# Kernel tuning notes

Measured on AMD Instinct MI355X. Metric: run time of the kernel, lower is better.

Reference implementation:

```python
import jax, jax.numpy as jnp
import numpy as np

B, S, D, H, DFF, E = 8, 1024, 1024, 16, 4096, 16
T = B * S
C = (2 * T) // E  # top-2 capacity, capacity_factor_eff = 1.0
EPS = 1.1920929e-07


def setup_inputs() -> dict:
    key = jax.random.key(0)
    ks = jax.random.split(key, 16)
    r = lambda k, shape, sc: jax.random.normal(k, shape, dtype=jnp.float32) * sc
    return {
        "x": r(ks[0], (B, S, D), 1.0),
        "in_proj_w": r(ks[1], (3 * D, D), 0.02),
        "in_proj_b": jnp.zeros((3 * D,), jnp.float32),
        "out_proj_w": r(ks[2], (D, D), 0.02),
        "out_proj_b": jnp.zeros((D,), jnp.float32),
        "ln1_g": jnp.ones((D,), jnp.float32),
        "ln1_b": jnp.zeros((D,), jnp.float32),
        "ln2_g": jnp.ones((D,), jnp.float32),
        "ln2_b": jnp.zeros((D,), jnp.float32),
        "wg": r(ks[3], (D, E), 0.02),
        "w1": r(ks[4], (E, D, DFF), 0.02),
        "b1": jnp.zeros((E, DFF), jnp.float32),
        "w2": r(ks[5], (E, DFF, D), 0.02),
        "b2": jnp.zeros((E, D), jnp.float32),
    }


def _layernorm(v, g, b):
    m = v.mean(-1, keepdims=True)
    var = ((v - m) ** 2).mean(-1, keepdims=True)
    return (v - m) * jax.lax.rsqrt(var + 1e-5) * g + b


def reference(x, in_proj_w, in_proj_b, out_proj_w, out_proj_b,
              ln1_g, ln1_b, ln2_g, ln2_b, wg, w1, b1, w2, b2):
    hd = D // H
    # ---- self-attention block (dropout=0, eval) ----
    qkv = x @ in_proj_w.T + in_proj_b          # [B,S,3D]
    q, k, v = jnp.split(qkv, 3, axis=-1)
    heads = lambda t: t.reshape(B, S, H, hd).transpose(0, 2, 1, 3)  # [B,H,S,hd]
    q, k, v = heads(q), heads(k), heads(v)
    att = jax.nn.softmax(jnp.einsum('bhqd,bhkd->bhqk', q, k) / np.float32(np.sqrt(hd)), axis=-1)
    o = jnp.einsum('bhqk,bhkd->bhqd', att, v).transpose(0, 2, 1, 3).reshape(B, S, D)
    o = o @ out_proj_w.T + out_proj_b
    x = _layernorm(x + o, ln1_g, ln1_b)
    # ---- top-2 MoE (GShard/deepspeed-style gating, no noise at eval) ----
    xt = x.reshape(T, D)
    logits = xt @ wg                                    # [T,E]
    gates = jax.nn.softmax(logits, axis=-1)
    idx1 = jnp.argmax(gates, axis=-1)
    m1 = jax.nn.one_hot(idx1, E, dtype=jnp.float32)
    logits2 = jnp.where(m1 > 0, -jnp.inf, logits)
    idx2 = jnp.argmax(logits2, axis=-1)
    m2 = jax.nn.one_hot(idx2, E, dtype=jnp.float32)
    loc1 = jnp.cumsum(m1, axis=0) - m1                  # position within expert for top-1
    loc2 = jnp.cumsum(m2, axis=0) - m2 + m1.sum(0, keepdims=True)
    m1 = m1 * (loc1 < C)                                # drop tokens over capacity
    m2 = m2 * (loc2 < C)
    p1 = (loc1 * m1).sum(-1).astype(jnp.int32)          # [T] capacity slot
    p2 = (loc2 * m2).sum(-1).astype(jnp.int32)
    g1 = (gates * m1).sum(-1)
    g2 = (gates * m2).sum(-1)
    denom = jnp.maximum(g1 + g2, EPS)
    g1, g2 = g1 / denom, g2 / denom
    keep1 = m1.sum(-1)                                  # 1.0 if kept else 0.0
    keep2 = m2.sum(-1)
    # dispatch: scatter tokens into [E, C, D] expert buffers
    buf = jnp.zeros((E, C, D), x.dtype)
    buf = buf.at[idx1, p1].add(xt * keep1[:, None]).at[idx2, p2].add(xt * keep2[:, None])
    # grouped expert FFN
    h = jax.nn.relu(jnp.einsum('ecd,edh->ech', buf, w1) + b1[:, None, :])
    y = jnp.einsum('ech,ehd->ecd', h, w2) + b2[:, None, :]
    # combine: gather back and weight by normalized gates (zero if dropped)
    moe_out = (g1 * keep1)[:, None] * y[idx1, p1] + (g2 * keep2)[:, None] * y[idx2, p2]
    x = _layernorm(x + moe_out.reshape(B, S, D), ln2_g, ln2_b)
    return x
```

## Files before the change

kernel.cpp:

```cpp
#include <hip/hip_runtime.h>
#include <cstdint>

#define DEVI __device__ __forceinline__

typedef short short8 __attribute__((ext_vector_type(8)));
typedef float f32x4 __attribute__((ext_vector_type(4)));
typedef unsigned short u16;
typedef u16 u16x4 __attribute__((ext_vector_type(4)));

static constexpr int Bz = 8, Ss = 1024, Dd = 1024, Hh = 16, HD = 64, DFF = 4096, Ee = 16;
static constexpr int Tt = Bz * Ss;
static constexpr int Cap = (2 * Tt) / Ee;
static constexpr int D3 = 3 * Dd;
static constexpr float EPSc = 1.1920929e-07f;
static constexpr size_t PT = (size_t)Tt * Dd;

DEVI u16 f2b(float f) {
    union { float f; uint32_t u; } v; v.f = f;
    return (u16)((v.u + 0x7FFFu + ((v.u >> 16) & 1u)) >> 16);
}
DEVI float b2f(u16 h) {
    union { uint32_t u; float f; } v; v.u = ((uint32_t)h) << 16; return v.f;
}
DEVI f32x4 zf4() { f32x4 v; v[0] = 0.f; v[1] = 0.f; v[2] = 0.f; v[3] = 0.f; return v; }

DEVI void gl16(const u16* g, u16* l) {
    __builtin_amdgcn_global_load_lds(
        (const __attribute__((address_space(1))) void*)g,
        (__attribute__((address_space(3))) void*)l, 16, 0, 0);
}

DEVI int swzb(int row, int col) {
    int byte = (row * 64 + col) * 2;
    byte ^= (row & 7) << 4;
    return byte >> 1;
}

__global__ __launch_bounds__(256)
void split3_kernel(const float* __restrict__ in, u16* __restrict__ out, long long n) {
    const long long i = ((long long)blockIdx.x * 256 + threadIdx.x) * 4;
    if (i >= n) return;
    const float4 v = *(const float4*)(in + i);
    const float f[4] = {v.x, v.y, v.z, v.w};
    u16x4 ph, pm, pl;
#pragma unroll
    for (int c = 0; c < 4; ++c) {
        const u16 hi = f2b(f[c]);
        const float r1 = f[c] - b2f(hi);
        const u16 mi = f2b(r1);
        const float r2 = r1 - b2f(mi);
        const u16 lo = f2b(r2);
        ph[c] = hi; pm[c] = mi; pl[c] = lo;
    }
    *(u16x4*)(out + i) = ph;
    *(u16x4*)(out + n + i) = pm;
    *(u16x4*)(out + 2 * n + i) = pl;
}

__global__ __launch_bounds__(256)
void tconv64_kernel(const float* __restrict__ in, u16* __restrict__ out, int R, int Cc) {
    __shared__ u16 tile[64][68];
    const int z = blockIdx.z;
    const int r0 = blockIdx.y * 64, c0 = blockIdx.x * 64;
    const int tr = threadIdx.x >> 4;
    const int tc4 = (threadIdx.x & 15) * 4;
    const float* ip = in + (size_t)z * R * Cc;
#pragma unroll
    for (int i = 0; i < 4; ++i) {
        const int row = tr + i * 16;
        const float4 v = *(const float4*)(ip + (size_t)(r0 + row) * Cc + c0 + tc4);
        u16x4 w;
        w[0] = f2b(v.x); w[1] = f2b(v.y); w[2] = f2b(v.z); w[3] = f2b(v.w);
        *(u16x4*)(&tile[row][tc4]) = w;
    }
    __syncthreads();
    u16* op = out + (size_t)z * R * Cc;
#pragma unroll
    for (int i = 0; i < 4; ++i) {
        const int orow = tr + i * 16;
        u16x4 w;
#pragma unroll
        for (int j = 0; j < 4; ++j) w[j] = tile[tc4 + j][orow];
        *(u16x4*)(op + (size_t)(c0 + orow) * R + r0 + tc4) = w;
    }
}

__global__ __launch_bounds__(256)
void vtrans_kernel(const u16* __restrict__ vh, const u16* __restrict__ vl,
                   u16* __restrict__ vth, u16* __restrict__ vtl) {
    __shared__ u16 th[32][33], tl[32][33];
    const int bh = blockIdx.z, d0 = blockIdx.y * 32, s0 = blockIdx.x * 32;
    const int bb = bh >> 4, hh = bh & 15;
    const int tr = threadIdx.x >> 5, tc = threadIdx.x & 31;
#pragma unroll
    for (int i = 0; i < 4; ++i) {
        const size_t src = (size_t)(bb * Ss + s0 + tr + i * 8) * Dd + hh * HD + d0 + tc;
        th[tr + i * 8][tc] = vh[src];
        tl[tr + i * 8][tc] = vl[src];
    }
    __syncthreads();
#pragma unroll
    for (int i = 0; i < 4; ++i) {
        const size_t dst = ((size_t)bh * HD + d0 + tr + i * 8) * Ss + s0 + tc;
        vth[dst] = th[tc][tr + i * 8];
        vtl[dst] = tl[tc][tr + i * 8];
    }
}

template <int SPLITS, int MODE>
__global__ __launch_bounds__(256)
void gemm_gl(const u16* __restrict__ A, const u16* __restrict__ Bt, void* __restrict__ Cout,
             const float* __restrict__ bias, int M, int N, int K,
             size_t psA, size_t psB,
             u16* __restrict__ qh, u16* __restrict__ ql,
             u16* __restrict__ kh, u16* __restrict__ kl,
             u16* __restrict__ vh, u16* __restrict__ vl) {
    __shared__ u16 As[SPLITS * 128 * 32];
    __shared__ u16 Bs[SPLITS * 128 * 32];
    const int tid = threadIdx.x;
    const int lane = tid & 63, wid = tid >> 6;
    const int wm = wid >> 1, wn = wid & 1;
    const int m0 = blockIdx.y * 128, n0 = blockIdx.x * 128;
    const int lr = lane & 15, lg = lane >> 4;
    const int lrow = lane >> 2;
    const int lcol = (lane & 3) * 8;

    f32x4 acc[4][4];
#pragma unroll
    for (int i = 0; i < 4; ++i)
#pragma unroll
        for (int j = 0; j < 4; ++j) acc[i][j] = zf4();

    for (int kt = 0; kt < K; kt += 32) {
#pragma unroll
        for (int p = 0; p < SPLITS; ++p) {
#pragma unroll
            for (int c = 0; c < 2; ++c) {
                const int r0 = wid * 32 + c * 16;
                gl16(A + p * psA + (size_t)(m0 + r0 + lrow) * K + kt + lcol,
                     As + p * 4096 + r0 * 32 + lane * 8);
                gl16(Bt + p * psB + (size_t)(n0 + r0 + lrow) * K + kt + lcol,
                     Bs + p * 4096 + r0 * 32 + lane * 8);
            }
        }
        __syncthreads();

        short8 af[SPLITS][4];
#pragma unroll
        for (int p = 0; p < SPLITS; ++p)
#pragma unroll
            for (int i = 0; i < 4; ++i)
                af[p][i] = *(const short8*)(As + p * 4096 + (wm * 64 + i * 16 + lr) * 32 + lg * 8);

#pragma unroll
        for (int bp = 0; bp < SPLITS; ++bp) {
            short8 bf[4];
#pragma unroll
            for (int j = 0; j < 4; ++j)
                bf[j] = *(const short8*)(Bs + bp * 4096 + (wn * 64 + j * 16 + lr) * 32 + lg * 8);
#pragma unroll
            for (int ap = 0; ap + bp < SPLITS; ++ap)
#pragma unroll
                for (int i = 0; i < 4; ++i)
#pragma unroll
                    for (int j = 0; j < 4; ++j)
                        acc[i][j] = __builtin_amdgcn_mfma_f32_16x16x32_bf16(af[ap][i], bf[j], acc[i][j], 0, 0, 0);
        }
        __syncthreads();
    }

    const int r4 = lg * 4;
    const int region = n0 >> 10;
#pragma unroll
    for (int j = 0; j < 4; ++j) {
        const int col = n0 + wn * 64 + j * 16 + lr;
        const float bv = bias[col];
#pragma unroll
        for (int i = 0; i < 4; ++i) {
#pragma unroll
            for (int r = 0; r < 4; ++r) {
                const int rowg = m0 + wm * 64 + i * 16 + r4 + r;
                float v = acc[i][j][r] + bv;
                if (MODE == 2) {
                    ((float*)Cout)[(size_t)rowg * N + col] = v;
                } else {
                    const size_t off = (size_t)rowg * Dd + (col & 1023);
                    if (region == 0) {
                        const float fs = v * 0.125f;
                        const u16 h = f2b(fs);
                        qh[off] = h; ql[off] = f2b(fs - b2f(h));
                    } else if (region == 1) {
                        const u16 h = f2b(v);
                        kh[off] = h; kl[off] = f2b(v - b2f(h));
                    } else {
                        const u16 h = f2b(v);
                        vh[off] = h; vl[off] = f2b(v - b2f(h));
                    }
                }
            }
        }
    }
}

template <int RELU>
__global__ __launch_bounds__(512)
void gemm_x2(const u16* __restrict__ A, const u16* __restrict__ Bt, u16* __restrict__ Cout,
             const float* __restrict__ bias, int M, int N, int K,
             size_t sA, size_t sB, size_t sC, int sBias) {
    __shared__ u16 lds[2][2][256 * 64];
    const int tid = threadIdx.x, lane = tid & 63, wid = tid >> 6;
    const int wm = wid >> 2, wn = wid & 3;
    const int lr = lane & 15, lg = lane >> 4;
    const int m0 = blockIdx.y * 256, n0 = blockIdx.x * 256;
    const int e = blockIdx.z;
    const u16* Ab = A + (size_t)e * sA;
    const u16* Bb = Bt + (size_t)e * sB;

    const int srow = wid * 8 + (lane >> 3);
    const int scol = (lane & 7) * 8;

    f32x4 acc[8][4];
#pragma unroll
    for (int i = 0; i < 8; ++i)
#pragma unroll
        for (int j = 0; j < 4; ++j) acc[i][j] = zf4();

#define STAGE_X2(b, kt)                                                              \
    {                                                                                \
        _Pragma("unroll")                                                            \
        for (int c = 0; c < 4; ++c)                                                  \
            gl16(Ab + (size_t)(m0 + c * 64 + srow) * K + (kt) + scol,                \
                 &lds[b][0][(c * 64 + srow) * 64 + scol]);                           \
        _Pragma("unroll")                                                            \
        for (int c = 0; c < 4; ++c)                                                  \
            gl16(Bb + (size_t)(n0 + c * 64 + srow) * K + (kt) + scol,                \
                 &lds[b][1][(c * 64 + srow) * 64 + scol]);                           \
    }

#define COMPUTE_X2(b)                                                                \
    {                                                                                \
        _Pragma("unroll")                                                            \
        for (int ks = 0; ks < 2; ++ks) {                                             \
            short8 af[8], bf[4];                                                     \
            _Pragma("unroll")                                                        \
            for (int i = 0; i < 8; ++i)                                              \
                af[i] = *(const short8*)(&lds[b][0][(wm * 128 + i * 16 + lr) * 64 + ks * 32 + lg * 8]); \
            _Pragma("unroll")                                                        \
            for (int j = 0; j < 4; ++j)                                              \
                bf[j] = *(const short8*)(&lds[b][1][(wn * 64 + j * 16 + lr) * 64 + ks * 32 + lg * 8]);  \
            _Pragma("unroll")                                                        \
            for (int i = 0; i < 8; ++i)                                              \
                _Pragma("unroll")                                                    \
                for (int j = 0; j < 4; ++j)                                          \
                    acc[i][j] = __builtin_amdgcn_mfma_f32_16x16x32_bf16(af[i], bf[j], acc[i][j], 0, 0, 0); \
        }                                                                            \
    }

    const int nt = K >> 6;
    STAGE_X2(0, 0)
    for (int t = 0; t < nt - 1; ++t) {
        const int cur = t & 1;
        STAGE_X2(cur ^ 1, (t + 1) * 64)
        asm volatile("s_waitcnt vmcnt(8)" ::: "memory");
        __builtin_amdgcn_s_barrier();
        COMPUTE_X2(cur)
        asm volatile("s_waitcnt lgkmcnt(0)" ::: "memory");
        __builtin_amdgcn_s_barrier();
    }
    asm volatile("s_waitcnt vmcnt(0)" ::: "memory");
    __builtin_amdgcn_s_barrier();
    COMPUTE_X2((nt - 1) & 1)

#undef STAGE_X2
#undef COMPUTE_X2

    const int r4 = lg * 4;
#pragma unroll
    for (int j = 0; j < 4; ++j) {
        const int col = n0 + wn * 64 + j * 16 + lr;
        const float bv = bias[(size_t)e * sBias + col];
#pragma unroll
        for (int i = 0; i < 8; ++i) {
#pragma unroll
            for (int r = 0; r < 4; ++r) {
                const int rowg = m0 + wm * 128 + i * 16 + r4 + r;
                float v = acc[i][j][r] + bv;
                if (RELU) v = fmaxf(v, 0.f);
                Cout[(size_t)e * sC + (size_t)rowg * N + col] = f2b(v);
            }
        }
    }
}

__global__ __launch_bounds__(256)
void attn_mfma(const u16* __restrict__ qhp, const u16* __restrict__ qlp,
               const u16* __restrict__ khp, const u16* __restrict__ klp,
               const u16* __restrict__ vthp, const u16* __restrict__ vtlp,
               u16* __restrict__ os) {
    __shared__ u16 Khi[64 * 64], Klo[64 * 64];
    __shared__ u16 Vhi[64 * 64], Vlo[64 * 64];
    __shared__ u16 Phi[4][16 * 64], Plo[4][16 * 64];

    const int qt = blockIdx.x, bh = blockIdx.y;
    const int bb = bh >> 4, hh = bh & 15;
    const int tid = threadIdx.x, lane = tid & 63, wid = tid >> 6;
    const int lr = lane & 15, lg = lane >> 4;

    short8 qhi[2], qlo[2];
    {
        const size_t qbase = (size_t)(bb * Ss + qt * 64 + wid * 16 + lr) * Dd + hh * HD;
#pragma unroll
        for (int ks = 0; ks < 2; ++ks) {
            qhi[ks] = *(const short8*)(qhp + qbase + ks * 32 + lg * 8);
            qlo[ks] = *(const short8*)(qlp + qbase + ks * 32 + lg * 8);
        }
    }

    float mrun[4], lrun[4];
    f32x4 oacc[4];
#pragma unroll
    for (int r = 0; r < 4; ++r) { mrun[r] = -1e30f; lrun[r] = 0.f; }
#pragma unroll
    for (int nf = 0; nf < 4; ++nf) oacc[nf] = zf4();

    const int srow = tid >> 2;
    const int sd = (tid & 3) * 16;

    u16* const PhiW = Phi[wid];
    u16* const PloW = Plo[wid];

    for (int kt = 0; kt < Ss / 64; ++kt) {
        const size_t krow = (size_t)(bb * Ss + kt * 64 + srow) * Dd + hh * HD + sd;
        const short8 k0 = *(const short8*)(khp + krow);
        const short8 k1 = *(const short8*)(khp + krow + 8);
        const short8 l0 = *(const short8*)(klp + krow);
        const short8 l1 = *(const short8*)(klp + krow + 8);
        const size_t vrow = ((size_t)bh * HD + srow) * Ss + kt * 64 + sd;
        const short8 v0 = *(const short8*)(vthp + vrow);
        const short8 v1 = *(const short8*)(vthp + vrow + 8);
        const short8 w0 = *(const short8*)(vtlp + vrow);
        const short8 w1 = *(const short8*)(vtlp + vrow + 8);
        __syncthreads();
        *(short8*)(Khi + swzb(srow, sd)) = k0;
        *(short8*)(Khi + swzb(srow, sd + 8)) = k1;
        *(short8*)(Klo + swzb(srow, sd)) = l0;
        *(short8*)(Klo + swzb(srow, sd + 8)) = l1;
        *(short8*)(Vhi + swzb(srow, sd)) = v0;
        *(short8*)(Vhi + swzb(srow, sd + 8)) = v1;
        *(short8*)(Vlo + swzb(srow, sd)) = w0;
        *(short8*)(Vlo + swzb(srow, sd + 8)) = w1;
        __syncthreads();

        f32x4 sc[4];
#pragma unroll
        for (int nf = 0; nf < 4; ++nf) sc[nf] = zf4();
#pragma unroll
        for (int nf = 0; nf < 4; ++nf)
#pragma unroll
            for (int ks = 0; ks < 2; ++ks) {
                const short8 kh = *(const short8*)(Khi + swzb(nf * 16 + lr, ks * 32 + lg * 8));
                const short8 kl = *(const short8*)(Klo + swzb(nf * 16 + lr, ks * 32 + lg * 8));
                sc[nf] = __builtin_amdgcn_mfma_f32_16x16x32_bf16(qhi[ks], kh, sc[nf], 0, 0, 0);
                sc[nf] = __builtin_amdgcn_mfma_f32_16x16x32_bf16(qhi[ks], kl, sc[nf], 0, 0, 0);
                sc[nf] = __builtin_amdgcn_mfma_f32_16x16x32_bf16(qlo[ks], kh, sc[nf], 0, 0, 0);
                sc[nf] = __builtin_amdgcn_mfma_f32_16x16x32_bf16(qlo[ks], kl, sc[nf], 0, 0, 0);
            }

        float scl[4];
#pragma unroll
        for (int r = 0; r < 4; ++r) {
            float m = fmaxf(fmaxf(sc[0][r], sc[1][r]), fmaxf(sc[2][r], sc[3][r]));
            m = fmaxf(m, __shfl_xor(m, 1));
            m = fmaxf(m, __shfl_xor(m, 2));
            m = fmaxf(m, __shfl_xor(m, 4));
            m = fmaxf(m, __shfl_xor(m, 8));
            const float mn = fmaxf(mrun[r], m);
            scl[r] = __expf(mrun[r] - mn);
            mrun[r] = mn;
            float s = 0.f;
#pragma unroll
            for (int nf = 0; nf < 4; ++nf) {
                const float p = __expf(sc[nf][r] - mn);
                sc[nf][r] = p;
                s += p;
            }
            s += __shfl_xor(s, 1);
            s += __shfl_xor(s, 2);
            s += __shfl_xor(s, 4);
            s += __shfl_xor(s, 8);
            lrun[r] = lrun[r] * scl[r] + s;
        }

#pragma unroll
        for (int nf = 0; nf < 4; ++nf)
#pragma unroll
            for (int r = 0; r < 4; ++r) {
                const float p = sc[nf][r];
                const u16 h = f2b(p);
                const int idx = swzb(lg * 4 + r, nf * 16 + lr);
                PhiW[idx] = h;
                PloW[idx] = f2b(p - b2f(h));
            }

#pragma unroll
        for (int nf = 0; nf < 4; ++nf)
#pragma unroll
            for (int r = 0; r < 4; ++r) oacc[nf][r] *= scl[r];

#pragma unroll
        for (int ks = 0; ks < 2; ++ks) {
            const short8 ph = *(const short8*)(PhiW + swzb(lr, ks * 32 + lg * 8));
            const short8 pl = *(const short8*)(PloW + swzb(lr, ks * 32 + lg * 8));
#pragma unroll
            for (int nf = 0; nf < 4; ++nf) {
                const short8 vh = *(const short8*)(Vhi + swzb(nf * 16 + lr, ks * 32 + lg * 8));
                const short8 vl = *(const short8*)(Vlo + swzb(nf * 16 + lr, ks * 32 + lg * 8));
                oacc[nf] = __builtin_amdgcn_mfma_f32_16x16x32_bf16(ph, vh, oacc[nf], 0, 0, 0);
                oacc[nf] = __builtin_amdgcn_mfma_f32_16x16x32_bf16(ph, vl, oacc[nf], 0, 0, 0);
                oacc[nf] = __builtin_amdgcn_mfma_f32_16x16x32_bf16(pl, vh, oacc[nf], 0, 0, 0);
                oacc[nf] = __builtin_amdgcn_mfma_f32_16x16x32_bf16(pl, vl, oacc[nf], 0, 0, 0);
            }
        }
    }

#pragma unroll
    for (int r = 0; r < 4; ++r) {
        const float inv = 1.f / lrun[r];
        const size_t base = (size_t)(bb * Ss + qt * 64 + wid * 16 + lg * 4 + r) * Dd + hh * HD;
#pragma unroll
        for (int nf = 0; nf < 4; ++nf) {
            const float o = oacc[nf][r] * inv;
            const u16 h = f2b(o);
            const float r1 = o - b2f(h);
            const u16 m = f2b(r1);
            const u16 l = f2b(r1 - b2f(m));
            const size_t off = base + nf * 16 + lr;
            os[off] = h;
            os[PT + off] = m;
            os[2 * PT + off] = l;
        }
    }
}

DEVI double block_reduce_d(double v, double* sred, int tid) {
#pragma unroll
    for (int off = 32; off > 0; off >>= 1) v += __shfl_down(v, off);
    __syncthreads();
    if ((tid & 63) == 0) sred[tid >> 6] = v;
    __syncthreads();
    return sred[0] + sred[1] + sred[2] + sred[3];
}

__global__ __launch_bounds__(256)
void ln1_kernel(const float* __restrict__ x, const float* __restrict__ ap,
                const float* __restrict__ g, const float* __restrict__ b,
                float* __restrict__ x1f) {
    __shared__ double sred[4];
    const int t = blockIdx.x, tid = threadIdx.x;
    const float4 xv = ((const float4*)(x + (size_t)t * Dd))[tid];
    const float4 av = ((const float4*)(ap + (size_t)t * Dd))[tid];
    const double v0 = (double)xv.x + (double)av.x;
    const double v1 = (double)xv.y + (double)av.y;
    const double v2 = (double)xv.z + (double)av.z;
    const double v3 = (double)xv.w + (double)av.w;
    const double s = block_reduce_d(v0 + v1 + v2 + v3, sred, tid);
    const double mean = s * (1.0 / Dd);
    const double c0 = v0 - mean, c1 = v1 - mean, c2 = v2 - mean, c3 = v3 - mean;
    const double s2 = block_reduce_d(c0 * c0 + c1 * c1 + c2 * c2 + c3 * c3, sred, tid);
    const double rstd = 1.0 / sqrt(s2 * (1.0 / Dd) + 1e-5);
    const float4 gv = ((const float4*)g)[tid];
    const float4 bv = ((const float4*)b)[tid];
    float4 ov;
    ov.x = (float)(c0 * rstd * (double)gv.x + (double)bv.x);
    ov.y = (float)(c1 * rstd * (double)gv.y + (double)bv.y);
    ov.z = (float)(c2 * rstd * (double)gv.z + (double)bv.z);
    ov.w = (float)(c3 * rstd * (double)gv.w + (double)bv.w);
    ((float4*)(x1f + (size_t)t * Dd))[tid] = ov;
}

__global__ __launch_bounds__(256)
void gate1_kernel(const float* __restrict__ x1f, const float* __restrict__ wg,
                  int* __restrict__ idx1, int* __restrict__ idx2,
                  float* __restrict__ gate1, float* __restrict__ gate2) {
    const int tid = threadIdx.x, lane = tid & 63, wid = tid >> 6;
    const int t = blockIdx.x * 4 + wid;
    double acc[16];
#pragma unroll
    for (int e = 0; e < 16; ++e) acc[e] = 0.0;
    for (int i = 0; i < 16; ++i) {
        const int d = i * 64 + lane;
        const double xv = (double)x1f[(size_t)t * Dd + d];
        const float4* wr = (const float4*)(wg + (size_t)d * 16);
        const float4 w0 = wr[0], w1 = wr[1], w2 = wr[2], w3 = wr[3];
        acc[0] += xv * (double)w0.x;  acc[1] += xv * (double)w0.y;
        acc[2] += xv * (double)w0.z;  acc[3] += xv * (double)w0.w;
        acc[4] += xv * (double)w1.x;  acc[5] += xv * (double)w1.y;
        acc[6] += xv * (double)w1.z;  acc[7] += xv * (double)w1.w;
        acc[8] += xv * (double)w2.x;  acc[9] += xv * (double)w2.y;
        acc[10] += xv * (double)w2.z; acc[11] += xv * (double)w2.w;
        acc[12] += xv * (double)w3.x; acc[13] += xv * (double)w3.y;
        acc[14] += xv * (double)w3.z; acc[15] += xv * (double)w3.w;
    }
#pragma unroll
    for (int e = 0; e < 16; ++e) {
        acc[e] += __shfl_xor(acc[e], 1);
        acc[e] += __shfl_xor(acc[e], 2);
        acc[e] += __shfl_xor(acc[e], 4);
        acc[e] += __shfl_xor(acc[e], 8);
        acc[e] += __shfl_xor(acc[e], 16);
        acc[e] += __shfl_xor(acc[e], 32);
    }
    if (lane == 0) {
        double mx = acc[0];
#pragma unroll
        for (int e = 1; e < 16; ++e) mx = fmax(mx, acc[e]);
        double z = 0.0, ex[16];
#pragma unroll
        for (int e = 0; e < 16; ++e) { ex[e] = exp(acc[e] - mx); z += ex[e]; }
        int b1 = 0; double v1 = acc[0];
#pragma unroll
        for (int e = 1; e < 16; ++e) if (acc[e] > v1) { v1 = acc[e]; b1 = e; }
        int b2 = (b1 == 0) ? 1 : 0; double v2 = acc[b2];
#pragma unroll
        for (int e = 0; e < 16; ++e) if (e != b1 && acc[e] > v2) { v2 = acc[e]; b2 = e; }
        const double rz = 1.0 / z;
        idx1[t] = b1; idx2[t] = b2;
        gate1[t] = (float)(ex[b1] * rz); gate2[t] = (float)(ex[b2] * rz);
    }
}

__global__ __launch_bounds__(256)
void gate2_kernel(const int* __restrict__ idx1, const int* __restrict__ idx2,
                  const float* __restrict__ gate1, const float* __restrict__ gate2,
                  int* __restrict__ p1, int* __restrict__ p2,
                  int* __restrict__ k1, int* __restrict__ k2,
                  float* __restrict__ w1, float* __restrict__ w2) {
    __shared__ int hist[16];
    __shared__ unsigned long long sb1[4][16], sb2[4][16];
    __shared__ int sbase1[16], sbase2[16];
    const int tid = threadIdx.x, lane = tid & 63, wid = tid >> 6;
    if (tid < 16) hist[tid] = 0;
    __syncthreads();
    for (int t = tid; t < Tt; t += 256) atomicAdd(&hist[idx1[t]], 1);
    __syncthreads();
    if (tid < 16) { sbase1[tid] = 0; sbase2[tid] = hist[tid]; }
    __syncthreads();
    const unsigned long long below = (1ULL << lane) - 1ULL;
    for (int ch = 0; ch < Tt / 256; ++ch) {
        const int t = ch * 256 + tid;
        const int a = idx1[t], b = idx2[t];
#pragma unroll
        for (int e = 0; e < 16; ++e) {
            const unsigned long long m1 = __ballot(a == e);
            const unsigned long long m2 = __ballot(b == e);
            if (lane == 0) { sb1[wid][e] = m1; sb2[wid][e] = m2; }
        }
        __syncthreads();
        int r1 = __popcll(sb1[wid][a] & below);
        int r2 = __popcll(sb2[wid][b] & below);
#pragma unroll
        for (int w = 0; w < 4; ++w)
            if (w < wid) { r1 += __popcll(sb1[w][a]); r2 += __popcll(sb2[w][b]); }
        const int loc1 = sbase1[a] + r1, loc2 = sbase2[b] + r2;
        const int kk1 = loc1 < Cap, kk2 = loc2 < Cap;
        const float g1 = kk1 ? gate1[t] : 0.f;
        const float g2 = kk2 ? gate2[t] : 0.f;
        const float dn = fmaxf(g1 + g2, EPSc);
        p1[t] = kk1 ? loc1 : 0;
        p2[t] = kk2 ? loc2 : 0;
        k1[t] = kk1; k2[t] = kk2;
        w1[t] = g1 / dn; w2[t] = g2 / dn;
        __syncthreads();
        if (tid == 0) {
#pragma unroll
            for (int e = 0; e < 16; ++e) {
                int c1 = 0, c2 = 0;
#pragma unroll
                for (int w = 0; w < 4; ++w) { c1 += __popcll(sb1[w][e]); c2 += __popcll(sb2[w][e]); }
                sbase1[e] += c1; sbase2[e] += c2;
            }
        }
        __syncthreads();
    }
}

__global__ __launch_bounds__(256)
void dispatch_kernel(const float* __restrict__ x1f,
                     const int* __restrict__ i1, const int* __restrict__ p1, const int* __restrict__ k1,
                     const int* __restrict__ i2, const int* __restrict__ p2, const int* __restrict__ k2,
                     u16* __restrict__ buf) {
    const int t = blockIdx.x, tid = threadIdx.x;
    const float4 v = ((const float4*)(x1f + (size_t)t * Dd))[tid];
    u16x4 pw;
    pw[0] = f2b(v.x); pw[1] = f2b(v.y); pw[2] = f2b(v.z); pw[3] = f2b(v.w);
    if (k1[t]) *(u16x4*)(buf + ((size_t)i1[t] * Cap + p1[t]) * Dd + tid * 4) = pw;
    if (k2[t]) *(u16x4*)(buf + ((size_t)i2[t] * Cap + p2[t]) * Dd + tid * 4) = pw;
}

__global__ __launch_bounds__(256)
void combine_ln2(const float* __restrict__ x1f, const u16* __restrict__ y,
                 const int* __restrict__ i1, const int* __restrict__ p1, const float* __restrict__ w1,
                 const int* __restrict__ i2, const int* __restrict__ p2, const float* __restrict__ w2,
                 const float* __restrict__ g, const float* __restrict__ b,
                 float* __restrict__ out) {
    __shared__ double sred[4];
    const int t = blockIdx.x, tid = threadIdx.x;
    const size_t r1 = ((size_t)i1[t] * Cap + p1[t]) * Dd;
    const size_t r2 = ((size_t)i2[t] * Cap + p2[t]) * Dd;
    const double a1 = (double)w1[t], a2 = (double)w2[t];
    const u16x4 y1 = *(const u16x4*)(y + r1 + tid * 4);
    const u16x4 y2 = *(const u16x4*)(y + r2 + tid * 4);
    const float4 xv = ((const float4*)(x1f + (size_t)t * Dd))[tid];
    const double v0 = (double)xv.x + a1 * (double)b2f(y1[0]) + a2 * (double)b2f(y2[0]);
    const double v1 = (double)xv.y + a1 * (double)b2f(y1[1]) + a2 * (double)b2f(y2[1]);
    const double v2 = (double)xv.z + a1 * (double)b2f(y1[2]) + a2 * (double)b2f(y2[2]);
    const double v3 = (double)xv.w + a1 * (double)b2f(y1[3]) + a2 * (double)b2f(y2[3]);
    const double s = block_reduce_d(v0 + v1 + v2 + v3, sred, tid);
    const double mean = s * (1.0 / Dd);
    const double c0 = v0 - mean, c1 = v1 - mean, c2 = v2 - mean, c3 = v3 - mean;
    const double s2 = block_reduce_d(c0 * c0 + c1 * c1 + c2 * c2 + c3 * c3, sred, tid);
    const double rstd = 1.0 / sqrt(s2 * (1.0 / Dd) + 1e-5);
    const float4 gv = ((const float4*)g)[tid];
    const float4 bv = ((const float4*)b)[tid];
    float4 ov;
    ov.x = (float)(c0 * rstd * (double)gv.x + (double)bv.x);
    ov.y = (float)(c1 * rstd * (double)gv.y + (double)bv.y);
    ov.z = (float)(c2 * rstd * (double)gv.z + (double)bv.z);
    ov.w = (float)(c3 * rstd * (double)gv.w + (double)bv.w);
    ((float4*)(out + (size_t)t * Dd))[tid] = ov;
}

extern "C" void kernel_launch(void* const* d_in, const int* in_sizes, int n_in,
                              void* d_out, int out_size, void* d_ws, size_t ws_size,
                              hipStream_t stream) {
    (void)in_sizes; (void)n_in; (void)out_size; (void)ws_size;
    const float* x    = (const float*)d_in[0];
    const float* inW  = (const float*)d_in[1];
    const float* inB  = (const float*)d_in[2];
    const float* outW = (const float*)d_in[3];
    const float* outB = (const float*)d_in[4];
    const float* ln1g = (const float*)d_in[5];
    const float* ln1b = (const float*)d_in[6];
    const float* ln2g = (const float*)d_in[7];
    const float* ln2b = (const float*)d_in[8];
    const float* wg   = (const float*)d_in[9];
    const float* w1   = (const float*)d_in[10];
    const float* b1   = (const float*)d_in[11];
    const float* w2   = (const float*)d_in[12];
    const float* b2   = (const float*)d_in[13];
    float* out = (float*)d_out;

    char* ws = (char*)d_ws;
    const size_t MB = 1024 * 1024;
    u16*   xs3   = (u16*)(ws + 0);
    u16*   inW3  = (u16*)(ws + 48 * MB);
    u16*   qh    = (u16*)(ws + 66 * MB);
    u16*   ql    = (u16*)(ws + 82 * MB);
    u16*   kh    = (u16*)(ws + 98 * MB);
    u16*   kl    = (u16*)(ws + 114 * MB);
    u16*   vh    = (u16*)(ws + 130 * MB);
    u16*   vl    = (u16*)(ws + 146 * MB);
    u16*   vth   = (u16*)(ws + 162 * MB);
    u16*   vtl   = (u16*)(ws + 178 * MB);
    u16*   os3   = (u16*)(ws + 194 * MB);
    u16*   outW3 = (u16*)(ws + 0);
    float* aproj = (float*)(ws + 6 * MB);
    u16*   wt    = (u16*)(ws + 0);
    u16*   hbuf  = (u16*)(ws + 128 * MB);
    u16*   ybuf  = (u16*)(ws + 256 * MB);
    u16*   ebuf  = (u16*)(ws + 288 * MB);
    float* x1f   = (float*)(ws + 320 * MB);
    char*  gbase = ws + 352 * MB;
    int*   idx1 = (int*)(gbase + 0 * Tt * 4);
    int*   idx2 = (int*)(gbase + 1 * Tt * 4);
    float* gt1  = (float*)(gbase + 2 * Tt * 4);
    float* gt2  = (float*)(gbase + 3 * Tt * 4);
    int*   p1   = (int*)(gbase + 4 * Tt * 4);
    int*   p2   = (int*)(gbase + 5 * Tt * 4);
    int*   k1   = (int*)(gbase + 6 * Tt * 4);
    int*   k2   = (int*)(gbase + 7 * Tt * 4);
    float* w1c  = (float*)(gbase + 8 * Tt * 4);
    float* w2c  = (float*)(gbase + 9 * Tt * 4);

    const long long nTD = (long long)Tt * Dd;
    const long long nW1 = (long long)D3 * Dd;
    const long long nW2 = (long long)Dd * Dd;

    split3_kernel<<<(int)(nTD / 1024), 256, 0, stream>>>(x, xs3, nTD);
    split3_kernel<<<(int)(nW1 / 1024), 256, 0, stream>>>(inW, inW3, nW1);
    gemm_gl<3, 3><<<dim3(D3 / 128, Tt / 128, 1), 256, 0, stream>>>(
        xs3, inW3, nullptr, inB, Tt, D3, Dd, (size_t)nTD, (size_t)nW1,
        qh, ql, kh, kl, vh, vl);
    vtrans_kernel<<<dim3(Ss / 32, HD / 32, Bz * Hh), 256, 0, stream>>>(vh, vl, vth, vtl);
    attn_mfma<<<dim3(Ss / 64, Bz * Hh), 256, 0, stream>>>(qh, ql, kh, kl, vth, vtl, os3);
    split3_kernel<<<(int)(nW2 / 1024), 256, 0, stream>>>(outW, outW3, nW2);
    gemm_gl<3, 2><<<dim3(Dd / 128, Tt / 128, 1), 256, 0, stream>>>(
        os3, outW3, aproj, outB, Tt, Dd, Dd, (size_t)nTD, (size_t)nW2,
        nullptr, nullptr, nullptr, nullptr, nullptr, nullptr);
    ln1_kernel<<<Tt, 256, 0, stream>>>(x, aproj, ln1g, ln1b, x1f);
    gate1_kernel<<<Tt / 4, 256, 0, stream>>>(x1f, wg, idx1, idx2, gt1, gt2);
    gate2_kernel<<<1, 256, 0, stream>>>(idx1, idx2, gt1, gt2, p1, p2, k1, k2, w1c, w2c);
    hipMemsetAsync(ebuf, 0, (size_t)Ee * Cap * Dd * 2, stream);
    dispatch_kernel<<<Tt, 256, 0, stream>>>(x1f, idx1, p1, k1, idx2, p2, k2, ebuf);
    tconv64_kernel<<<dim3(DFF / 64, Dd / 64, Ee), 256, 0, stream>>>(w1, wt, Dd, DFF);
    gemm_x2<1><<<dim3(DFF / 256, Cap / 256, Ee), 512, 0, stream>>>(
        ebuf, wt, hbuf, b1, Cap, DFF, Dd,
        (size_t)Cap * Dd, (size_t)DFF * Dd, (size_t)Cap * DFF, DFF);
    tconv64_kernel<<<dim3(Dd / 64, DFF / 64, Ee), 256, 0, stream>>>(w2, wt, DFF, Dd);
    gemm_x2<0><<<dim3(Dd / 256, Cap / 256, Ee), 512, 0, stream>>>(
        hbuf, wt, ybuf, b2, Cap, Dd, DFF,
        (size_t)Cap * DFF, (size_t)Dd * DFF, (size_t)Cap * Dd, Dd);
    combine_ln2<<<Tt, 256, 0, stream>>>(x1f, ybuf, idx1, p1, w1c, idx2, p2, w2c, ln2g, ln2b, out);
}
```

Measured before the change: 1.367 ms.

## Double-buffer 3-way split bf16 GEMM with 512-thread blocks

Replaces the single-buffered 256-thread split-precision GEMM used for the QKV and output projections with a 512-thread version that double-buffers the LDS tiles. The next K-slice is loaded directly to shared memory while the current one is multiplied, synchronised with explicit vmcnt waits and barriers. Each of the eight waves now owns a 32x64 output sub-tile instead of 64x64, which lowers per-thread accumulator pressure. The cost is twice the LDS (96KB per block), which may limit blocks per CU, and more barrier traffic per K step.

```diff
diff --git a/kernel.cpp b/kernel.cpp
--- a/kernel.cpp
+++ b/kernel.cpp
@@ -107,67 +107,91 @@
     }
 }
 
-template <int SPLITS, int MODE>
-__global__ __launch_bounds__(256)
-void gemm_gl(const u16* __restrict__ A, const u16* __restrict__ Bt, void* __restrict__ Cout,
+template <int MODE>
+__global__ __launch_bounds__(512)
+void gemm_x3(const u16* __restrict__ A, const u16* __restrict__ Bt, void* __restrict__ Cout,
              const float* __restrict__ bias, int M, int N, int K,
              size_t psA, size_t psB,
              u16* __restrict__ qh, u16* __restrict__ ql,
              u16* __restrict__ kh, u16* __restrict__ kl,
              u16* __restrict__ vh, u16* __restrict__ vl) {
-    __shared__ u16 As[SPLITS * 128 * 32];
-    __shared__ u16 Bs[SPLITS * 128 * 32];
-    const int tid = threadIdx.x;
-    const int lane = tid & 63, wid = tid >> 6;
+    __shared__ u16 lds[2 * 3 * 2 * 128 * 32];
+    const int tid = threadIdx.x, lane = tid & 63, wid = tid >> 6;
     const int wm = wid >> 1, wn = wid & 1;
+    const int lr = lane & 15, lg = lane >> 4;
     const int m0 = blockIdx.y * 128, n0 = blockIdx.x * 128;
-    const int lr = lane & 15, lg = lane >> 4;
-    const int lrow = lane >> 2;
-    const int lcol = (lane & 3) * 8;
-
-    f32x4 acc[4][4];
-#pragma unroll
-    for (int i = 0; i < 4; ++i)
+
+    const u16* gsrc[6];
+    int ldof[6];
+#pragma unroll
+    for (int c = 0; c < 6; ++c) {
+        const int g = wid * 6 + c;
+        const int p = g >> 4, r = g & 15, mat = r >> 3, seg = r & 7;
+        const int row = seg * 16 + (lane >> 2);
+        const int col = (lane & 3) * 8;
+        gsrc[c] = (mat ? Bt + p * psB + (size_t)(n0 + row) * K
+                       : A + p * psA + (size_t)(m0 + row) * K) + col;
+        ldof[c] = (p * 2 + mat) * 4096 + seg * 512 + lane * 8;
+    }
+
+    f32x4 acc[2][4];
+#pragma unroll
+    for (int i = 0; i < 2; ++i)
 #pragma unroll
         for (int j = 0; j < 4; ++j) acc[i][j] = zf4();
 
-    for (int kt = 0; kt < K; kt += 32) {
-#pragma unroll
-        for (int p = 0; p < SPLITS; ++p) {
-#pragma unroll
-            for (int c = 0; c < 2; ++c) {
-                const int r0 = wid * 32 + c * 16;
-                gl16(A + p * psA + (size_t)(m0 + r0 + lrow) * K + kt + lcol,
-                     As + p * 4096 + r0 * 32 + lane * 8);
-                gl16(Bt + p * psB + (size_t)(n0 + r0 + lrow) * K + kt + lcol,
-                     Bs + p * 4096 + r0 * 32 + lane * 8);
-            }
-        }
-        __syncthreads();
-
-        short8 af[SPLITS][4];
-#pragma unroll
-        for (int p = 0; p < SPLITS; ++p)
-#pragma unroll
-            for (int i = 0; i < 4; ++i)
-                af[p][i] = *(const short8*)(As + p * 4096 + (wm * 64 + i * 16 + lr) * 32 + lg * 8);
-
-#pragma unroll
-        for (int bp = 0; bp < SPLITS; ++bp) {
-            short8 bf[4];
-#pragma unroll
-            for (int j = 0; j < 4; ++j)
-                bf[j] = *(const short8*)(Bs + bp * 4096 + (wn * 64 + j * 16 + lr) * 32 + lg * 8);
-#pragma unroll
-            for (int ap = 0; ap + bp < SPLITS; ++ap)
-#pragma unroll
-                for (int i = 0; i < 4; ++i)
-#pragma unroll
-                    for (int j = 0; j < 4; ++j)
-                        acc[i][j] = __builtin_amdgcn_mfma_f32_16x16x32_bf16(af[ap][i], bf[j], acc[i][j], 0, 0, 0);
-        }
-        __syncthreads();
-    }
+#define STAGE_X3(b, kto)                                                       \
+    {                                                                          \
+        _Pragma("unroll")                                                      \
+        for (int c = 0; c < 6; ++c)                                            \
+            gl16(gsrc[c] + (kto), lds + (b) * 24576 + ldof[c]);                \
+    }
+
+#define COMPUTE_X3(b)                                                          \
+    {                                                                          \
+        const u16* L = lds + (b) * 24576;                                      \
+        short8 af[3][2];                                                       \
+        _Pragma("unroll")                                                      \
+        for (int p = 0; p < 3; ++p)                                            \
+            _Pragma("unroll")                                                  \
+            for (int i = 0; i < 2; ++i)                                        \
+                af[p][i] = *(const short8*)(L + (p * 2) * 4096 +               \
+                                            (wm * 32 + i * 16 + lr) * 32 + lg * 8); \
+        _Pragma("unroll")                                                      \
+        for (int bp = 0; bp < 3; ++bp) {                                       \
+            short8 bf[4];                                                      \
+            _Pragma("unroll")                                                  \
+            for (int j = 0; j < 4; ++j)                                        \
+                bf[j] = *(const short8*)(L + (bp * 2 + 1) * 4096 +             \
+                                         (wn * 64 + j * 16 + lr) * 32 + lg * 8); \
+            _Pragma("unroll")                                                  \
+            for (int ap = 0; ap + bp < 3; ++ap)                                \
+                _Pragma("unroll")                                              \
+                for (int i = 0; i < 2; ++i)                                    \
+                    _Pragma("unroll")                                          \
+                    for (int j = 0; j < 4; ++j)                                \
+                        acc[i][j] = __builtin_amdgcn_mfma_f32_16x16x32_bf16(   \
+                            af[ap][i], bf[j], acc[i][j], 0, 0, 0);             \
+        }                                                                      \
+    }
+
+    const int nt = K >> 5;
+    STAGE_X3(0, 0)
+    for (int t = 0; t < nt - 1; ++t) {
+        const int cur = t & 1;
+        STAGE_X3(cur ^ 1, (t + 1) * 32)
+        asm volatile("s_waitcnt vmcnt(6)" ::: "memory");
+        __builtin_amdgcn_s_barrier();
+        COMPUTE_X3(cur)
+        asm volatile("s_waitcnt lgkmcnt(0)" ::: "memory");
+        __builtin_amdgcn_s_barrier();
+    }
+    asm volatile("s_waitcnt vmcnt(0)" ::: "memory");
+    __builtin_amdgcn_s_barrier();
+    COMPUTE_X3((nt - 1) & 1)
+
+#undef STAGE_X3
+#undef COMPUTE_X3
 
     const int r4 = lg * 4;
     const int region = n0 >> 10;
@@ -176,10 +200,10 @@
         const int col = n0 + wn * 64 + j * 16 + lr;
         const float bv = bias[col];
 #pragma unroll
-        for (int i = 0; i < 4; ++i) {
+        for (int i = 0; i < 2; ++i) {
 #pragma unroll
             for (int r = 0; r < 4; ++r) {
-                const int rowg = m0 + wm * 64 + i * 16 + r4 + r;
+                const int rowg = m0 + wm * 32 + i * 16 + r4 + r;
                 float v = acc[i][j][r] + bv;
                 if (MODE == 2) {
                     ((float*)Cout)[(size_t)rowg * N + col] = v;
@@ -688,13 +712,13 @@
 
     split3_kernel<<<(int)(nTD / 1024), 256, 0, stream>>>(x, xs3, nTD);
     split3_kernel<<<(int)(nW1 / 1024), 256, 0, stream>>>(inW, inW3, nW1);
-    gemm_gl<3, 3><<<dim3(D3 / 128, Tt / 128, 1), 256, 0, stream>>>(
+    gemm_x3<3><<<dim3(D3 / 128, Tt / 128, 1), 512, 0, stream>>>(
         xs3, inW3, nullptr, inB, Tt, D3, Dd, (size_t)nTD, (size_t)nW1,
         qh, ql, kh, kl, vh, vl);
     vtrans_kernel<<<dim3(Ss / 32, HD / 32, Bz * Hh), 256, 0, stream>>>(vh, vl, vth, vtl);
     attn_mfma<<<dim3(Ss / 64, Bz * Hh), 256, 0, stream>>>(qh, ql, kh, kl, vth, vtl, os3);
     split3_kernel<<<(int)(nW2 / 1024), 256, 0, stream>>>(outW, outW3, nW2);
-    gemm_gl<3, 2><<<dim3(Dd / 128, Tt / 128, 1), 256, 0, stream>>>(
+    gemm_x3<2><<<dim3(Dd / 128, Tt / 128, 1), 512, 0, stream>>>(
         os3, outW3, aproj, outB, Tt, Dd, Dd, (size_t)nTD, (size_t)nW2,
         nullptr, nullptr, nullptr, nullptr, nullptr, nullptr);
     ln1_kernel<<<Tt, 256, 0, stream>>>(x, aproj, ln1g, ln1b, x1f);
```

Result: no change. 1.342 ms (-1.8%).
